# Kernel optimization log

Hardware: AMD Instinct MI355X
Metric: run time of the kernel (lower is better)

Reference implementation:

```python
import jax, jax.numpy as jnp
import numpy as np
import math

T, B, C, F, H, LF, GF = 1024, 8, 512, 64, 8, 64, 64


def setup_inputs() -> dict:
    key = jax.random.key(0)
    ks = jax.random.split(key, 24)
    s = 0.02  # weight init scale for stability through the recurrence
    rn = lambda k, shp, sc=1.0: jax.random.normal(k, shp, jnp.float32) * sc
    inp = {
        "x": rn(ks[0], (B, T, C)),
        "ln_g": jnp.ones((C,), jnp.float32),
        "ln_b": jnp.zeros((C,), jnp.float32),
        "tl_initial": rn(ks[1], (C,)),
        "tl_premix": jax.random.uniform(ks[2], (C,), jnp.float32),
        "tl_w1": rn(ks[3], (C, LF), s), "tl_b1": jnp.zeros((LF,), jnp.float32),
        "tl_w2": rn(ks[4], (LF, C), s), "tl_b2": jnp.zeros((C,), jnp.float32),
        "bias": jnp.zeros((C,), jnp.float32),
        "gating_res": jax.random.uniform(ks[5], (C,), jnp.float32),
        "g_w1": rn(ks[6], (C, GF), s), "g_b1": jnp.zeros((GF,), jnp.float32),
        "g_w2": rn(ks[7], (GF, C), s), "g_b2": jnp.zeros((C,), jnp.float32),
        "dn_initial": rn(ks[8], (H, F, F)),
        "A_w": rn(ks[9], (H, C, F), s), "A_b": rn(ks[10], (H, F), s),
        "B_w": jnp.zeros((H, C, F), jnp.float32), "B_b": rn(ks[11], (H, F), s),
        "C_w": rn(ks[12], (H, C, F), s), "C_b": rn(ks[13], (H, F), s),
        "D_w": rn(ks[14], (H, C, F), s), "D_b": rn(ks[15], (H, F), s),
        "I_w": rn(ks[16], (H, C, F), s), "I_b": rn(ks[17], (H, F), s),
        "S_w": rn(ks[18], (H, C, F), s), "S_b": rn(ks[19], (H, F), s),
        "O_w": rn(ks[20], (H, F, C), s),
    }
    return inp


def _deltanet_head(y, init_state, Aw, Ab, Bw, Bb, Cw, Cb, Dw, Db, Iw, Ib, Sw, Sb, Ow):
    # y: [T, B, C]; init_state: [F, F]
    f = init_state.shape[-1]
    sf = math.sqrt(f)  # awk_safe
    a = y @ Aw + Ab   # [T,B,F]
    b = y @ Bw + Bb
    c = y @ Cw + Cb
    d = y @ Dw + Db
    i = y @ Iw + Ib
    sel = y @ Sw + Sb
    st0 = jnp.broadcast_to(init_state, (y.shape[1], f, f)).astype(y.dtype)

    def step(st, ins):
        sel_t, a_t, b_t, c_t, d_t, i_t = ins  # each [B,F]
        st = (st * jax.nn.sigmoid(i_t)[:, None, :]
              + jnp.einsum('bij,bj->bi', st, a_t)[:, :, None] * b_t[:, None, :] / sf
              + c_t[:, :, None] * d_t[:, None, :])
        out = jnp.einsum('bf,bfg->bg', sel_t, st)
        return st, out

    st, o = jax.lax.scan(step, st0, (sel, a, b, c, d, i))
    return o @ Ow, st  # [T,B,C]


def reference(x, ln_g, ln_b, tl_initial, tl_premix, tl_w1, tl_b1, tl_w2, tl_b2,
              bias, gating_res, g_w1, g_b1, g_w2, g_b2, dn_initial,
              A_w, A_b, B_w, B_b, C_w, C_b, D_w, D_b, I_w, I_b, S_w, S_b, O_w):
    xt = jnp.swapaxes(x, 0, -2)  # [T, B, C] (time_dim=-2)
    res = xt
    # LayerNorm (eps=1e-5)
    mu = jnp.mean(xt, -1, keepdims=True)
    var = jnp.mean((xt - mu) ** 2, -1, keepdims=True)
    h = (xt - mu) / jnp.sqrt(var + 1e-5) * ln_g + ln_b
    # TokenLerp (state=None -> xf[0]=initial)
    xf = jnp.concatenate([jnp.broadcast_to(tl_initial, (1,) + h.shape[1:]).astype(h.dtype), h[:-1]], axis=0)
    pm = h + (xf - h) * tl_premix
    decide = jax.nn.sigmoid(jax.nn.gelu(pm @ tl_w1 + tl_b1, approximate=False) @ tl_w2 + tl_b2)
    h = h + (xf - h) * decide
    # y starts from bias; heads are chained sequentially (y feeds next head)
    y = jnp.broadcast_to(bias, h.shape).astype(h.dtype)
    for k in range(dn_initial.shape[0]):
        y, _ = _deltanet_head(y, dn_initial[k], A_w[k], A_b[k], B_w[k], B_b[k],
                              C_w[k], C_b[k], D_w[k], D_b[k], I_w[k], I_b[k],
                              S_w[k], S_b[k], O_w[k])
    gate = jax.nn.sigmoid(jax.nn.gelu((y + h * gating_res) @ g_w1 + g_b1, approximate=False) @ g_w2 + g_b2)
    # use_residual=True path: returns res + y (no transpose back, matching source)
    return res + y * gate
```

## Files before the change

### kernel.cpp

```cpp
#include <hip/hip_runtime.h>
#include <hip/hip_bf16.h>

#define T_DIM 1024
#define B_DIM 8
#define C_DIM 512
#define F_DIM 64
#define H_DIM 8
#define CHUNK 32
#define NCHUNK 32

__device__ __forceinline__ float sigmoidf_(float v) { return 1.0f / (1.0f + __expf(-v)); }
__device__ __forceinline__ float geluf_(float v) { return 0.5f * v * (1.0f + erff(v * 0.70710678118654752f)); }
__device__ __forceinline__ float rl_(float v, int l) {
  return __uint_as_float(__builtin_amdgcn_readlane(__float_as_uint(v), l));
}

struct GemmArgs {
  const float* A; const float* W; const float* bias; float* out;
  int M, K, N;
  const float* x; const float* mu; const float* rstd;
  const float* ln_g; const float* ln_b; const float* tl_initial; const float* premix;
  const float* yv; const float* gres;
  float* h2;
  const float* Wg[6]; const float* bg[6];
};

struct AFetch {
  float4 v0, v1, v2, v3, v4;
  float s0, s1, s2, s3;
};

template<int MODE_A>
__device__ __forceinline__ AFetch a_fetch(const GemmArgs& g, int r, int c) {
  AFetch f; f.s0 = f.s1 = f.s2 = f.s3 = 0.f;
  if (MODE_A == 0) {
    f.v0 = *(const float4*)&g.A[r * g.K + c];
  } else if (MODE_A == 1) {
    const int b = r & 7, t = r >> 3;
    f.v0 = *(const float4*)&g.x[(b * T_DIM + t) * C_DIM + c];
    f.s0 = g.mu[r]; f.s1 = g.rstd[r];
    if (t > 0) {
      f.v1 = *(const float4*)&g.x[(b * T_DIM + t - 1) * C_DIM + c];
      f.s2 = g.mu[r - 8]; f.s3 = g.rstd[r - 8];
    } else {
      f.v1 = *(const float4*)&g.tl_initial[c];
    }
    f.v2 = *(const float4*)&g.ln_g[c];
    f.v3 = *(const float4*)&g.ln_b[c];
    f.v4 = *(const float4*)&g.premix[c];
  } else {
    f.v0 = *(const float4*)&g.yv[(r >> 3) * C_DIM + c];
    f.v1 = *(const float4*)&g.h2[r * C_DIM + c];
    f.v2 = *(const float4*)&g.gres[c];
  }
  return f;
}

template<int MODE_A>
__device__ __forceinline__ float4 a_combine(const AFetch& f, int r) {
  if (MODE_A == 0) return f.v0;
  float4 o;
  float* op = (float*)&o;
  const float* xa = (const float*)&f.v0;
  const float* xb = (const float*)&f.v1;
  const float* lg = (const float*)&f.v2;
  const float* lb = (const float*)&f.v3;
  const float* pm = (const float*)&f.v4;
  if (MODE_A == 1) {
    const int t = r >> 3;
    #pragma unroll
    for (int q = 0; q < 4; ++q) {
      float h  = (xa[q] - f.s0) * f.s1 * lg[q] + lb[q];
      float xf = (t == 0) ? xb[q] : (xb[q] - f.s2) * f.s3 * lg[q] + lb[q];
      op[q] = h + (xf - h) * pm[q];
    }
    return o;
  }
  #pragma unroll
  for (int q = 0; q < 4; ++q)
    op[q] = xa[q] + xb[q] * lg[q];
  return o;
}

template<int MODE_B>
__device__ __forceinline__ float4 w_fetch(const GemmArgs& g, int kk, int n0, int tc) {
  if (MODE_B == 1)
    return *(const float4*)&g.Wg[blockIdx.y][kk * 64 + (tc << 2)];
  return *(const float4*)&g.W[kk * g.N + n0 + (tc << 2)];
}

template<int MODE_A, int MODE_B, int EPI>
__global__ __launch_bounds__(256) void gemm_kernel(GemmArgs g) {
  __shared__ float AsT[16][68];
  __shared__ float Bs[16][64];
  const int m0 = blockIdx.x * 64, n0 = blockIdx.y * 64;
  const int tid = threadIdx.x;
  const int tr = tid >> 4, tc = tid & 15;
  const int ai = tid >> 2, aj = (tid & 3) << 2;
  const float scg = (MODE_B == 1 && blockIdx.y == 1) ? 0.125f : 1.0f;
  float acc[4][4] = {};
  AFetch fa = a_fetch<MODE_A>(g, m0 + ai, aj);
  float4 wv = w_fetch<MODE_B>(g, tr, n0, tc);
  for (int k0 = 0; k0 < g.K; k0 += 16) {
    if (k0) __syncthreads();
    const float4 av = a_combine<MODE_A>(fa, m0 + ai);
    AsT[aj + 0][ai] = av.x;
    AsT[aj + 1][ai] = av.y;
    AsT[aj + 2][ai] = av.z;
    AsT[aj + 3][ai] = av.w;
    *(float4*)&Bs[tr][tc << 2] =
        make_float4(wv.x * scg, wv.y * scg, wv.z * scg, wv.w * scg);
    if (k0 + 16 < g.K) {
      fa = a_fetch<MODE_A>(g, m0 + ai, k0 + 16 + aj);
      wv = w_fetch<MODE_B>(g, k0 + 16 + tr, n0, tc);
    }
    __syncthreads();
    #pragma unroll
    for (int kk = 0; kk < 16; ++kk) {
      const float4 a4 = *(const float4*)&AsT[kk][tr << 2];
      const float4 b4 = *(const float4*)&Bs[kk][tc << 2];
      const float avr[4] = {a4.x, a4.y, a4.z, a4.w};
      const float bvr[4] = {b4.x, b4.y, b4.z, b4.w};
      #pragma unroll
      for (int r_ = 0; r_ < 4; ++r_)
        #pragma unroll
        for (int c_ = 0; c_ < 4; ++c_)
          acc[r_][c_] = fmaf(avr[r_], bvr[c_], acc[r_][c_]);
    }
  }
  #pragma unroll
  for (int r_ = 0; r_ < 4; ++r_) {
    const int rr = m0 + (tr << 2) + r_;
    #pragma unroll
    for (int c_ = 0; c_ < 4; ++c_) {
      const int lc = (tc << 2) + c_;
      const int cc = n0 + lc;
      float v = acc[r_][c_];
      if (MODE_B == 1) v += g.bg[blockIdx.y][lc] * scg;
      else if (g.bias) v += g.bias[cc];
      if (EPI == 0) {
        g.out[rr * g.N + cc] = v;
      } else if (EPI == 1) {
        g.out[rr * g.N + cc] = geluf_(v);
      } else if (EPI == 2) {
        float d = sigmoidf_(v);
        const int b = rr & 7, t = rr >> 3;
        float xv = g.x[(b * T_DIM + t) * C_DIM + cc];
        float h = (xv - g.mu[rr]) * g.rstd[rr] * g.ln_g[cc] + g.ln_b[cc];
        float xf;
        if (t == 0) xf = g.tl_initial[cc];
        else {
          float xp = g.x[(b * T_DIM + t - 1) * C_DIM + cc];
          xf = (xp - g.mu[rr - 8]) * g.rstd[rr - 8] * g.ln_g[cc] + g.ln_b[cc];
        }
        g.h2[rr * C_DIM + cc] = h + (xf - h) * d;
      } else {
        float gate = sigmoidf_(v);
        const int b = rr & 7, t = rr >> 3;
        float res = g.x[(b * T_DIM + t) * C_DIM + cc];
        g.out[rr * C_DIM + cc] = res + g.yv[t * C_DIM + cc] * gate;
      }
    }
  }
}

__global__ __launch_bounds__(256) void ln_stats_kernel(const float* __restrict__ x,
                                                       float* __restrict__ mu,
                                                       float* __restrict__ rstd) {
  const int row = blockIdx.x * 4 + (threadIdx.x >> 6);
  const int lane = threadIdx.x & 63;
  const int b = row & 7, t = row >> 3;
  const float* xr = x + (b * T_DIM + t) * C_DIM;
  float4 v0 = *(const float4*)&xr[lane * 8];
  float4 v1 = *(const float4*)&xr[lane * 8 + 4];
  float s  = v0.x + v0.y + v0.z + v0.w + v1.x + v1.y + v1.z + v1.w;
  float s2 = v0.x*v0.x + v0.y*v0.y + v0.z*v0.z + v0.w*v0.w
           + v1.x*v1.x + v1.y*v1.y + v1.z*v1.z + v1.w*v1.w;
  #pragma unroll
  for (int m = 1; m < 64; m <<= 1) { s += __shfl_xor(s, m); s2 += __shfl_xor(s2, m); }
  if (lane == 0) {
    float mean = s * (1.0f / 512.0f);
    float var = s2 * (1.0f / 512.0f) - mean * mean;
    mu[row] = mean;
    rstd[row] = rsqrtf(var + 1e-5f);
  }
}

__global__ __launch_bounds__(256) void yinit_kernel(const float* __restrict__ bias,
                                                    float* __restrict__ y) {
  int i = blockIdx.x * blockDim.x + threadIdx.x;
  y[i] = bias[i & (C_DIM - 1)];
}


__global__ __launch_bounds__(256) void scan_phaseA(const float* __restrict__ PRJ,
                                                   float* __restrict__ chPT,
                                                   float* __restrict__ chS) {
  const int j = blockIdx.x;
  const int tid = threadIdx.x;
  const int ri = tid >> 4, ci = tid & 15;
  float Pm[4][4], Sm[4][4];
  #pragma unroll
  for (int r = 0; r < 4; ++r)
    #pragma unroll
    for (int c = 0; c < 4; ++c) {
      Pm[r][c] = (ri * 4 + r == ci * 4 + c) ? 1.0f : 0.0f;
      Sm[r][c] = 0.0f;
    }
  const float* base = PRJ + j * CHUNK * 384;
  float4 pa = *(const float4*)&base[      ci * 4];
  float4 pb = *(const float4*)&base[ 64 + ci * 4];
  float4 pc = *(const float4*)&base[128 + ri * 4];
  float4 pd = *(const float4*)&base[192 + ci * 4];
  float4 pi = *(const float4*)&base[256 + ci * 4];
  for (int s = 0; s < CHUNK; ++s) {
    float4 na = pa, nb = pb, nc2 = pc, nd = pd, ni = pi;
    if (s + 1 < CHUNK) {
      const float* b2 = base + (s + 1) * 384;
      na  = *(const float4*)&b2[      ci * 4];
      nb  = *(const float4*)&b2[ 64 + ci * 4];
      nc2 = *(const float4*)&b2[128 + ri * 4];
      nd  = *(const float4*)&b2[192 + ci * 4];
      ni  = *(const float4*)&b2[256 + ci * 4];
    }
    const float sg[4] = {sigmoidf_(pi.x), sigmoidf_(pi.y), sigmoidf_(pi.z), sigmoidf_(pi.w)};
    const float aa[4] = {pa.x, pa.y, pa.z, pa.w};
    const float bb[4] = {pb.x, pb.y, pb.z, pb.w};
    const float cv[4] = {pc.x, pc.y, pc.z, pc.w};
    const float dd[4] = {pd.x, pd.y, pd.z, pd.w};
    float rp[4], rs[4];
    #pragma unroll
    for (int r = 0; r < 4; ++r) {
      rp[r] = Pm[r][0]*aa[0] + Pm[r][1]*aa[1] + Pm[r][2]*aa[2] + Pm[r][3]*aa[3];
      rs[r] = Sm[r][0]*aa[0] + Sm[r][1]*aa[1] + Sm[r][2]*aa[2] + Sm[r][3]*aa[3];
    }
    #pragma unroll
    for (int m = 1; m <= 8; m <<= 1) {
      #pragma unroll
      for (int r = 0; r < 4; ++r) {
        rp[r] += __shfl_xor(rp[r], m);
        rs[r] += __shfl_xor(rs[r], m);
      }
    }
    #pragma unroll
    for (int r = 0; r < 4; ++r)
      #pragma unroll
      for (int c = 0; c < 4; ++c) {
        Pm[r][c] = Pm[r][c] * sg[c] + rp[r] * bb[c];
        Sm[r][c] = Sm[r][c] * sg[c] + rs[r] * bb[c] + cv[r] * dd[c];
      }
    pa = na; pb = nb; pc = nc2; pd = nd; pi = ni;
  }
  float* cpT = chPT + j * 4096;
  float* cs  = chS + j * 4096;
  #pragma unroll
  for (int c = 0; c < 4; ++c)
    *(float4*)&cpT[(ci*4+c)*64 + ri*4] =
        make_float4(Pm[0][c], Pm[1][c], Pm[2][c], Pm[3][c]);
  #pragma unroll
  for (int r = 0; r < 4; ++r)
    *(float4*)&cs[(ri*4+r)*64 + ci*4] = make_float4(Sm[r][0], Sm[r][1], Sm[r][2], Sm[r][3]);
}

__device__ __forceinline__ float cstep(const float4 (&P)[16], float sv, float rv) {
  float p0 = 0.f, p1 = 0.f, p2 = 0.f, p3 = 0.f;
  #pragma unroll
  for (int q = 0; q < 16; ++q) {
    p0 = fmaf(rl_(rv, q * 4 + 0), P[q].x, p0);
    p1 = fmaf(rl_(rv, q * 4 + 1), P[q].y, p1);
    p2 = fmaf(rl_(rv, q * 4 + 2), P[q].z, p2);
    p3 = fmaf(rl_(rv, q * 4 + 3), P[q].w, p3);
  }
  return sv + ((p0 + p1) + (p2 + p3));
}

__global__ __launch_bounds__(64) void scan_combine(const float* __restrict__ st0,
                                                   const float* __restrict__ chPT,
                                                   const float* __restrict__ chS,
                                                   float* __restrict__ bnd) {
  const int lane = threadIdx.x;
  const int r = blockIdx.x;
  float rv = st0[r * 64 + lane];
  const float* basePT = chPT + lane * 64;
  const float* baseS  = chS + r * 64 + lane;
  float* bndRL = bnd + r * 64 + lane;
  for (int j = 0; j < NCHUNK; ++j) {
    float4 P[16];
    const float* pp = basePT + j * 4096;
    #pragma unroll
    for (int q = 0; q < 16; ++q) P[q] = *(const float4*)&pp[q * 4];
    const float sv = baseS[j * 4096];
    bndRL[j * 4096] = rv;
    rv = cstep(P, sv, rv);
  }
}

__global__ __launch_bounds__(256) void scan_phaseC(const float* __restrict__ PRJ,
                                                   const float* __restrict__ bnd,
                                                   const float* __restrict__ Ow,
                                                   float* __restrict__ y) {
  __shared__ float olds[CHUNK][4][64];
  __shared__ float osT[64][CHUNK + 1];
  const int j = blockIdx.x;
  const int tid = threadIdx.x;
  const int ri = tid >> 4, ci = tid & 15, w = tid >> 6;
  float st[4][4];
  #pragma unroll
  for (int r = 0; r < 4; ++r) {
    const float4 v = *(const float4*)&bnd[j*4096 + (ri*4+r)*64 + ci*4];
    st[r][0] = v.x; st[r][1] = v.y; st[r][2] = v.z; st[r][3] = v.w;
  }
  const float* base = PRJ + j * CHUNK * 384;
  float4 pa = *(const float4*)&base[      ci * 4];
  float4 pb = *(const float4*)&base[ 64 + ci * 4];
  float4 pc = *(const float4*)&base[128 + ri * 4];
  float4 pd = *(const float4*)&base[192 + ci * 4];
  float4 pi = *(const float4*)&base[256 + ci * 4];
  float4 ps = *(const float4*)&base[320 + ri * 4];
  for (int s = 0; s < CHUNK; ++s) {
    float4 na = pa, nb = pb, nc2 = pc, nd = pd, ni = pi, ns = ps;
    if (s + 1 < CHUNK) {
      const float* b2 = base + (s + 1) * 384;
      na  = *(const float4*)&b2[      ci * 4];
      nb  = *(const float4*)&b2[ 64 + ci * 4];
      nc2 = *(const float4*)&b2[128 + ri * 4];
      nd  = *(const float4*)&b2[192 + ci * 4];
      ni  = *(const float4*)&b2[256 + ci * 4];
      ns  = *(const float4*)&b2[320 + ri * 4];
    }
    const float sg[4] = {sigmoidf_(pi.x), sigmoidf_(pi.y), sigmoidf_(pi.z), sigmoidf_(pi.w)};
    const float aa[4] = {pa.x, pa.y, pa.z, pa.w};
    const float bb[4] = {pb.x, pb.y, pb.z, pb.w};
    const float cv[4] = {pc.x, pc.y, pc.z, pc.w};
    const float dd[4] = {pd.x, pd.y, pd.z, pd.w};
    const float ss[4] = {ps.x, ps.y, ps.z, ps.w};
    float rd[4];
    #pragma unroll
    for (int r = 0; r < 4; ++r)
      rd[r] = st[r][0]*aa[0] + st[r][1]*aa[1] + st[r][2]*aa[2] + st[r][3]*aa[3];
    #pragma unroll
    for (int m = 1; m <= 8; m <<= 1) {
      #pragma unroll
      for (int r = 0; r < 4; ++r) rd[r] += __shfl_xor(rd[r], m);
    }
    float po[4] = {0.f, 0.f, 0.f, 0.f};
    #pragma unroll
    for (int r = 0; r < 4; ++r)
      #pragma unroll
      for (int c = 0; c < 4; ++c) {
        const float nv = st[r][c] * sg[c] + rd[r] * bb[c] + cv[r] * dd[c];
        st[r][c] = nv;
        po[c] = fmaf(ss[r], nv, po[c]);
      }
    #pragma unroll
    for (int c = 0; c < 4; ++c) {
      po[c] += __shfl_xor(po[c], 16);
      po[c] += __shfl_xor(po[c], 32);
    }
    if ((tid & 48) == 0)
      *(float4*)&olds[s][w][ci * 4] = make_float4(po[0], po[1], po[2], po[3]);
    pa = na; pb = nb; pc = nc2; pd = nd; pi = ni; ps = ns;
  }
  __syncthreads();
  #pragma unroll
  for (int e = 0; e < 8; ++e) {
    const int id = tid + 256 * e;
    const int f = id & 63, t = id >> 6;
    osT[f][t] = olds[t][0][f] + olds[t][1][f] + olds[t][2][f] + olds[t][3][f];
  }
  __syncthreads();
  const int c0 = tid << 1;
  float2 acc[CHUNK];
  #pragma unroll
  for (int t = 0; t < CHUNK; ++t) acc[t] = make_float2(0.f, 0.f);
  #pragma unroll 1
  for (int fo = 0; fo < 8; ++fo) {
    float2 ow[8];
    #pragma unroll
    for (int q = 0; q < 8; ++q)
      ow[q] = *(const float2*)&Ow[(fo * 8 + q) * C_DIM + c0];
    #pragma unroll
    for (int q = 0; q < 8; ++q) {
      const int f = fo * 8 + q;
      #pragma unroll
      for (int t8 = 0; t8 < 8; ++t8) {
        const float4 ov = *(const float4*)&osT[f][t8 * 4];
        acc[t8*4+0].x = fmaf(ov.x, ow[q].x, acc[t8*4+0].x);
        acc[t8*4+0].y = fmaf(ov.x, ow[q].y, acc[t8*4+0].y);
        acc[t8*4+1].x = fmaf(ov.y, ow[q].x, acc[t8*4+1].x);
        acc[t8*4+1].y = fmaf(ov.y, ow[q].y, acc[t8*4+1].y);
        acc[t8*4+2].x = fmaf(ov.z, ow[q].x, acc[t8*4+2].x);
        acc[t8*4+2].y = fmaf(ov.z, ow[q].y, acc[t8*4+2].y);
        acc[t8*4+3].x = fmaf(ov.w, ow[q].x, acc[t8*4+3].x);
        acc[t8*4+3].y = fmaf(ov.w, ow[q].y, acc[t8*4+3].y);
      }
    }
  }
  #pragma unroll
  for (int t = 0; t < CHUNK; ++t)
    *(float2*)&y[(j * CHUNK + t) * C_DIM + c0] = acc[t];
}

extern "C" void kernel_launch(void* const* d_in, const int* in_sizes, int n_in,
                              void* d_out, int out_size, void* d_ws, size_t ws_size,
                              hipStream_t stream) {
  const float* x       = (const float*)d_in[0];
  const float* ln_g    = (const float*)d_in[1];
  const float* ln_b    = (const float*)d_in[2];
  const float* tl_init = (const float*)d_in[3];
  const float* premix  = (const float*)d_in[4];
  const float* tl_w1   = (const float*)d_in[5];
  const float* tl_b1   = (const float*)d_in[6];
  const float* tl_w2   = (const float*)d_in[7];
  const float* tl_b2   = (const float*)d_in[8];
  const float* bias    = (const float*)d_in[9];
  const float* gres    = (const float*)d_in[10];
  const float* g_w1    = (const float*)d_in[11];
  const float* g_b1    = (const float*)d_in[12];
  const float* g_w2    = (const float*)d_in[13];
  const float* g_b2    = (const float*)d_in[14];
  const float* dn_init = (const float*)d_in[15];
  const float* A_w     = (const float*)d_in[16];
  const float* A_b     = (const float*)d_in[17];
  const float* B_w     = (const float*)d_in[18];
  const float* B_b     = (const float*)d_in[19];
  const float* C_w     = (const float*)d_in[20];
  const float* C_b     = (const float*)d_in[21];
  const float* D_w     = (const float*)d_in[22];
  const float* D_b     = (const float*)d_in[23];
  const float* I_w     = (const float*)d_in[24];
  const float* I_b     = (const float*)d_in[25];
  const float* S_w     = (const float*)d_in[26];
  const float* S_b     = (const float*)d_in[27];
  const float* O_w     = (const float*)d_in[28];

  float* ws      = (float*)d_ws;
  float* mu      = ws;
  float* rstd    = mu + 8192;
  float* hidden1 = rstd + 8192;
  float* y       = hidden1 + 524288;
  float* PRJ     = y + 524288;
  float* chPT    = PRJ + 393216;
  float* chS     = chPT + 131072;
  float* bnd     = chS + 131072;
  float* h2      = (float*)d_out;

  ln_stats_kernel<<<2048, 256, 0, stream>>>(x, mu, rstd);
  yinit_kernel<<<2048, 256, 0, stream>>>(bias, y);

  GemmArgs ga = {};
  ga.x = x; ga.mu = mu; ga.rstd = rstd; ga.ln_g = ln_g; ga.ln_b = ln_b;
  ga.tl_initial = tl_init; ga.premix = premix; ga.gres = gres; ga.h2 = h2;

  {
    GemmArgs g = ga; g.W = tl_w1; g.bias = tl_b1; g.out = hidden1;
    g.M = 8192; g.K = 512; g.N = 64;
    gemm_kernel<1, 0, 1><<<dim3(128, 1), 256, 0, stream>>>(g);
  }
  {
    GemmArgs g = ga; g.A = hidden1; g.W = tl_w2; g.bias = tl_b2;
    g.M = 8192; g.K = 64; g.N = 512;
    gemm_kernel<0, 0, 2><<<dim3(128, 8), 256, 0, stream>>>(g);
  }

  for (int k = 0; k < H_DIM; ++k) {
    {
      GemmArgs g = ga; g.A = y; g.out = PRJ; g.M = 1024; g.K = 512; g.N = 384;
      const int woff = k * C_DIM * F_DIM, boff = k * F_DIM;
      g.Wg[0] = A_w + woff; g.Wg[1] = B_w + woff; g.Wg[2] = C_w + woff;
      g.Wg[3] = D_w + woff; g.Wg[4] = I_w + woff; g.Wg[5] = S_w + woff;
      g.bg[0] = A_b + boff; g.bg[1] = B_b + boff; g.bg[2] = C_b + boff;
      g.bg[3] = D_b + boff; g.bg[4] = I_b + boff; g.bg[5] = S_b + boff;
      gemm_kernel<0, 1, 0><<<dim3(16, 6), 256, 0, stream>>>(g);
    }
    scan_phaseA<<<NCHUNK, 256, 0, stream>>>(PRJ, chPT, chS);
    scan_combine<<<64, 64, 0, stream>>>(dn_init + k * 4096, chPT, chS, bnd);
    scan_phaseC<<<NCHUNK, 256, 0, stream>>>(PRJ, bnd, O_w + k * F_DIM * C_DIM, y);
  }

  {
    GemmArgs g = ga; g.yv = y; g.W = g_w1; g.bias = g_b1; g.out = hidden1;
    g.M = 8192; g.K = 512; g.N = 64;
    gemm_kernel<2, 0, 1><<<dim3(128, 1), 256, 0, stream>>>(g);
  }
  {
    GemmArgs g = ga; g.yv = y; g.A = hidden1; g.W = g_w2; g.bias = g_b2;
    g.out = (float*)d_out; g.M = 8192; g.K = 64; g.N = 512;
    gemm_kernel<0, 0, 3><<<dim3(128, 8), 256, 0, stream>>>(g);
  }
}
```

Before: 968.0 us.

## Fuse MLP GEMM pairs, fuse head projection into scan phase A, merge y init

The two-layer MLPs (token-lerp decide and output gate) now run as one kernel per MLP. The 64-wide hidden activation stays in shared memory and each block loops over all 512 output columns, which removes the hidden1 round trip and a launch. Each head's projection GEMM is folded into scan_phaseA, so every chunk block computes its own 32x384 projections into LDS before scanning. The y bias initialization is merged into ln_stats. The cost is that projection now runs on only 32 blocks instead of 96, and the second MLP GEMM runs on 128 blocks instead of 1024, which lowers parallelism.

```diff
diff --git a/kernel.cpp b/kernel.cpp
--- a/kernel.cpp
+++ b/kernel.cpp
@@ -16,13 +16,12 @@
 }
 
 struct GemmArgs {
-  const float* A; const float* W; const float* bias; float* out;
-  int M, K, N;
+  const float* W; const float* bias; const float* W2; const float* bias2;
+  float* out;
   const float* x; const float* mu; const float* rstd;
   const float* ln_g; const float* ln_b; const float* tl_initial; const float* premix;
   const float* yv; const float* gres;
   float* h2;
-  const float* Wg[6]; const float* bg[6];
 };
 
 struct AFetch {
@@ -33,9 +32,7 @@
 template<int MODE_A>
 __device__ __forceinline__ AFetch a_fetch(const GemmArgs& g, int r, int c) {
   AFetch f; f.s0 = f.s1 = f.s2 = f.s3 = 0.f;
-  if (MODE_A == 0) {
-    f.v0 = *(const float4*)&g.A[r * g.K + c];
-  } else if (MODE_A == 1) {
+  if (MODE_A == 1) {
     const int b = r & 7, t = r >> 3;
     f.v0 = *(const float4*)&g.x[(b * T_DIM + t) * C_DIM + c];
     f.s0 = g.mu[r]; f.s1 = g.rstd[r];
@@ -58,7 +55,6 @@
 
 template<int MODE_A>
 __device__ __forceinline__ float4 a_combine(const AFetch& f, int r) {
-  if (MODE_A == 0) return f.v0;
   float4 o;
   float* op = (float*)&o;
   const float* xa = (const float*)&f.v0;
@@ -82,43 +78,61 @@
   return o;
 }
 
-template<int MODE_B>
-__device__ __forceinline__ float4 w_fetch(const GemmArgs& g, int kk, int n0, int tc) {
-  if (MODE_B == 1)
-    return *(const float4*)&g.Wg[blockIdx.y][kk * 64 + (tc << 2)];
-  return *(const float4*)&g.W[kk * g.N + n0 + (tc << 2)];
-}
-
-template<int MODE_A, int MODE_B, int EPI>
-__global__ __launch_bounds__(256) void gemm_kernel(GemmArgs g) {
+template<int MODE_A, int EPI>
+__global__ __launch_bounds__(256) void mlp_fused_kernel(GemmArgs g) {
   __shared__ float AsT[16][68];
   __shared__ float Bs[16][64];
-  const int m0 = blockIdx.x * 64, n0 = blockIdx.y * 64;
+  __shared__ float hT[64][68];
+  const int m0 = blockIdx.x * 64;
   const int tid = threadIdx.x;
   const int tr = tid >> 4, tc = tid & 15;
   const int ai = tid >> 2, aj = (tid & 3) << 2;
-  const float scg = (MODE_B == 1 && blockIdx.y == 1) ? 0.125f : 1.0f;
-  float acc[4][4] = {};
-  AFetch fa = a_fetch<MODE_A>(g, m0 + ai, aj);
-  float4 wv = w_fetch<MODE_B>(g, tr, n0, tc);
-  for (int k0 = 0; k0 < g.K; k0 += 16) {
-    if (k0) __syncthreads();
-    const float4 av = a_combine<MODE_A>(fa, m0 + ai);
-    AsT[aj + 0][ai] = av.x;
-    AsT[aj + 1][ai] = av.y;
-    AsT[aj + 2][ai] = av.z;
-    AsT[aj + 3][ai] = av.w;
-    *(float4*)&Bs[tr][tc << 2] =
-        make_float4(wv.x * scg, wv.y * scg, wv.z * scg, wv.w * scg);
-    if (k0 + 16 < g.K) {
-      fa = a_fetch<MODE_A>(g, m0 + ai, k0 + 16 + aj);
-      wv = w_fetch<MODE_B>(g, k0 + 16 + tr, n0, tc);
+  {
+    float acc[4][4] = {};
+    AFetch fa = a_fetch<MODE_A>(g, m0 + ai, aj);
+    float4 wv = *(const float4*)&g.W[tr * 64 + (tc << 2)];
+    for (int k0 = 0; k0 < 512; k0 += 16) {
+      if (k0) __syncthreads();
+      const float4 av = a_combine<MODE_A>(fa, m0 + ai);
+      AsT[aj + 0][ai] = av.x;
+      AsT[aj + 1][ai] = av.y;
+      AsT[aj + 2][ai] = av.z;
+      AsT[aj + 3][ai] = av.w;
+      *(float4*)&Bs[tr][tc << 2] = wv;
+      if (k0 + 16 < 512) {
+        fa = a_fetch<MODE_A>(g, m0 + ai, k0 + 16 + aj);
+        wv = *(const float4*)&g.W[(k0 + 16 + tr) * 64 + (tc << 2)];
+      }
+      __syncthreads();
+      #pragma unroll
+      for (int kk = 0; kk < 16; ++kk) {
+        const float4 a4 = *(const float4*)&AsT[kk][tr << 2];
+        const float4 b4 = *(const float4*)&Bs[kk][tc << 2];
+        const float avr[4] = {a4.x, a4.y, a4.z, a4.w};
+        const float bvr[4] = {b4.x, b4.y, b4.z, b4.w};
+        #pragma unroll
+        for (int r_ = 0; r_ < 4; ++r_)
+          #pragma unroll
+          for (int c_ = 0; c_ < 4; ++c_)
+            acc[r_][c_] = fmaf(avr[r_], bvr[c_], acc[r_][c_]);
+      }
     }
     __syncthreads();
     #pragma unroll
-    for (int kk = 0; kk < 16; ++kk) {
-      const float4 a4 = *(const float4*)&AsT[kk][tr << 2];
-      const float4 b4 = *(const float4*)&Bs[kk][tc << 2];
+    for (int r_ = 0; r_ < 4; ++r_)
+      #pragma unroll
+      for (int c_ = 0; c_ < 4; ++c_) {
+        const int cc = (tc << 2) + c_;
+        hT[cc][(tr << 2) + r_] = geluf_(acc[r_][c_] + g.bias[cc]);
+      }
+  }
+  __syncthreads();
+  for (int n0 = 0; n0 < 512; n0 += 64) {
+    float acc[4][4] = {};
+    #pragma unroll 4
+    for (int kk = 0; kk < 64; ++kk) {
+      const float4 a4 = *(const float4*)&hT[kk][tr << 2];
+      const float4 b4 = *(const float4*)&g.W2[kk * 512 + n0 + (tc << 2)];
       const float avr[4] = {a4.x, a4.y, a4.z, a4.w};
       const float bvr[4] = {b4.x, b4.y, b4.z, b4.w};
       #pragma unroll
@@ -127,38 +141,31 @@
         for (int c_ = 0; c_ < 4; ++c_)
           acc[r_][c_] = fmaf(avr[r_], bvr[c_], acc[r_][c_]);
     }
-  }
-  #pragma unroll
-  for (int r_ = 0; r_ < 4; ++r_) {
-    const int rr = m0 + (tr << 2) + r_;
-    #pragma unroll
-    for (int c_ = 0; c_ < 4; ++c_) {
-      const int lc = (tc << 2) + c_;
-      const int cc = n0 + lc;
-      float v = acc[r_][c_];
-      if (MODE_B == 1) v += g.bg[blockIdx.y][lc] * scg;
-      else if (g.bias) v += g.bias[cc];
-      if (EPI == 0) {
-        g.out[rr * g.N + cc] = v;
-      } else if (EPI == 1) {
-        g.out[rr * g.N + cc] = geluf_(v);
-      } else if (EPI == 2) {
-        float d = sigmoidf_(v);
-        const int b = rr & 7, t = rr >> 3;
-        float xv = g.x[(b * T_DIM + t) * C_DIM + cc];
-        float h = (xv - g.mu[rr]) * g.rstd[rr] * g.ln_g[cc] + g.ln_b[cc];
-        float xf;
-        if (t == 0) xf = g.tl_initial[cc];
-        else {
-          float xp = g.x[(b * T_DIM + t - 1) * C_DIM + cc];
-          xf = (xp - g.mu[rr - 8]) * g.rstd[rr - 8] * g.ln_g[cc] + g.ln_b[cc];
+    #pragma unroll
+    for (int r_ = 0; r_ < 4; ++r_) {
+      const int rr = m0 + (tr << 2) + r_;
+      #pragma unroll
+      for (int c_ = 0; c_ < 4; ++c_) {
+        const int cc = n0 + (tc << 2) + c_;
+        float v = acc[r_][c_] + g.bias2[cc];
+        if (EPI == 2) {
+          float d = sigmoidf_(v);
+          const int b = rr & 7, t = rr >> 3;
+          float xv = g.x[(b * T_DIM + t) * C_DIM + cc];
+          float h = (xv - g.mu[rr]) * g.rstd[rr] * g.ln_g[cc] + g.ln_b[cc];
+          float xf;
+          if (t == 0) xf = g.tl_initial[cc];
+          else {
+            float xp = g.x[(b * T_DIM + t - 1) * C_DIM + cc];
+            xf = (xp - g.mu[rr - 8]) * g.rstd[rr - 8] * g.ln_g[cc] + g.ln_b[cc];
+          }
+          g.h2[rr * C_DIM + cc] = h + (xf - h) * d;
+        } else {
+          float gate = sigmoidf_(v);
+          const int b = rr & 7, t = rr >> 3;
+          float res = g.x[(b * T_DIM + t) * C_DIM + cc];
+          g.out[rr * C_DIM + cc] = res + g.yv[t * C_DIM + cc] * gate;
         }
-        g.h2[rr * C_DIM + cc] = h + (xf - h) * d;
-      } else {
-        float gate = sigmoidf_(v);
-        const int b = rr & 7, t = rr >> 3;
-        float res = g.x[(b * T_DIM + t) * C_DIM + cc];
-        g.out[rr * C_DIM + cc] = res + g.yv[t * C_DIM + cc] * gate;
       }
     }
   }
@@ -166,7 +173,11 @@
 
 __global__ __launch_bounds__(256) void ln_stats_kernel(const float* __restrict__ x,
                                                        float* __restrict__ mu,
-                                                       float* __restrict__ rstd) {
+                                                       float* __restrict__ rstd,
+                                                       const float* __restrict__ bias,
+                                                       float* __restrict__ y) {
+  const int gid = blockIdx.x * 256 + threadIdx.x;
+  y[gid] = bias[gid & (C_DIM - 1)];
   const int row = blockIdx.x * 4 + (threadIdx.x >> 6);
   const int lane = threadIdx.x & 63;
   const int b = row & 7, t = row >> 3;
@@ -186,18 +197,62 @@
   }
 }
 
-__global__ __launch_bounds__(256) void yinit_kernel(const float* __restrict__ bias,
-                                                    float* __restrict__ y) {
-  int i = blockIdx.x * blockDim.x + threadIdx.x;
-  y[i] = bias[i & (C_DIM - 1)];
-}
-
-
-__global__ __launch_bounds__(256) void scan_phaseA(const float* __restrict__ PRJ,
-                                                   float* __restrict__ chPT,
-                                                   float* __restrict__ chS) {
+
+struct ProjAArgs {
+  const float* y; float* PRJ; float* chPT; float* chS;
+  const float* Wg[6]; const float* bg[6];
+};
+
+__global__ __launch_bounds__(256) void projA_kernel(ProjAArgs a) {
+  __shared__ float prjS[32][388];
+  __shared__ float ys[16][36];
+  __shared__ float Bs2[16][64];
   const int j = blockIdx.x;
+  const int R0 = j * CHUNK;
   const int tid = threadIdx.x;
+  {
+    const int rq = tid >> 5, ct = tid & 31;
+    const int srow = tid >> 3, sfq = tid & 7;
+    const int wkk = tid >> 4, wc4 = (tid & 15) << 2;
+    for (int grp = 0; grp < 6; ++grp) {
+      const float* W = a.Wg[grp];
+      const float scg = (grp == 1) ? 0.125f : 1.0f;
+      float acc[4][2] = {};
+      for (int k0 = 0; k0 < 512; k0 += 16) {
+        if (sfq < 4) {
+          const float4 v = *(const float4*)&a.y[(R0 + srow) * C_DIM + k0 + sfq * 4];
+          ys[sfq * 4 + 0][srow] = v.x; ys[sfq * 4 + 1][srow] = v.y;
+          ys[sfq * 4 + 2][srow] = v.z; ys[sfq * 4 + 3][srow] = v.w;
+        }
+        const float4 wv = *(const float4*)&W[(k0 + wkk) * 64 + wc4];
+        *(float4*)&Bs2[wkk][wc4] =
+            make_float4(wv.x * scg, wv.y * scg, wv.z * scg, wv.w * scg);
+        __syncthreads();
+        #pragma unroll
+        for (int kk = 0; kk < 16; ++kk) {
+          const float4 a4 = *(const float4*)&ys[kk][rq << 2];
+          const float2 b2 = *(const float2*)&Bs2[kk][ct << 1];
+          const float avr[4] = {a4.x, a4.y, a4.z, a4.w};
+          #pragma unroll
+          for (int r_ = 0; r_ < 4; ++r_) {
+            acc[r_][0] = fmaf(avr[r_], b2.x, acc[r_][0]);
+            acc[r_][1] = fmaf(avr[r_], b2.y, acc[r_][1]);
+          }
+        }
+        __syncthreads();
+      }
+      const float* bb = a.bg[grp];
+      const float b0 = bb[ct * 2] * scg, b1 = bb[ct * 2 + 1] * scg;
+      #pragma unroll
+      for (int r_ = 0; r_ < 4; ++r_) {
+        const int row = rq * 4 + r_;
+        const float2 o = make_float2(acc[r_][0] + b0, acc[r_][1] + b1);
+        *(float2*)&prjS[row][grp * 64 + ct * 2] = o;
+        *(float2*)&a.PRJ[(R0 + row) * 384 + grp * 64 + ct * 2] = o;
+      }
+      __syncthreads();
+    }
+  }
   const int ri = tid >> 4, ci = tid & 15;
   float Pm[4][4], Sm[4][4];
   #pragma unroll
@@ -207,25 +262,15 @@
       Pm[r][c] = (ri * 4 + r == ci * 4 + c) ? 1.0f : 0.0f;
       Sm[r][c] = 0.0f;
     }
-  const float* base = PRJ + j * CHUNK * 384;
-  float4 pa = *(const float4*)&base[      ci * 4];
-  float4 pb = *(const float4*)&base[ 64 + ci * 4];
-  float4 pc = *(const float4*)&base[128 + ri * 4];
-  float4 pd = *(const float4*)&base[192 + ci * 4];
-  float4 pi = *(const float4*)&base[256 + ci * 4];
   for (int s = 0; s < CHUNK; ++s) {
-    float4 na = pa, nb = pb, nc2 = pc, nd = pd, ni = pi;
-    if (s + 1 < CHUNK) {
-      const float* b2 = base + (s + 1) * 384;
-      na  = *(const float4*)&b2[      ci * 4];
-      nb  = *(const float4*)&b2[ 64 + ci * 4];
-      nc2 = *(const float4*)&b2[128 + ri * 4];
-      nd  = *(const float4*)&b2[192 + ci * 4];
-      ni  = *(const float4*)&b2[256 + ci * 4];
-    }
+    const float4 pa = *(const float4*)&prjS[s][      ci * 4];
+    const float4 pb = *(const float4*)&prjS[s][ 64 + ci * 4];
+    const float4 pc = *(const float4*)&prjS[s][128 + ri * 4];
+    const float4 pd = *(const float4*)&prjS[s][192 + ci * 4];
+    const float4 pi = *(const float4*)&prjS[s][256 + ci * 4];
     const float sg[4] = {sigmoidf_(pi.x), sigmoidf_(pi.y), sigmoidf_(pi.z), sigmoidf_(pi.w)};
     const float aa[4] = {pa.x, pa.y, pa.z, pa.w};
-    const float bb[4] = {pb.x, pb.y, pb.z, pb.w};
+    const float bb2[4] = {pb.x, pb.y, pb.z, pb.w};
     const float cv[4] = {pc.x, pc.y, pc.z, pc.w};
     const float dd[4] = {pd.x, pd.y, pd.z, pd.w};
     float rp[4], rs[4];
@@ -246,13 +291,12 @@
     for (int r = 0; r < 4; ++r)
       #pragma unroll
       for (int c = 0; c < 4; ++c) {
-        Pm[r][c] = Pm[r][c] * sg[c] + rp[r] * bb[c];
-        Sm[r][c] = Sm[r][c] * sg[c] + rs[r] * bb[c] + cv[r] * dd[c];
-      }
-    pa = na; pb = nb; pc = nc2; pd = nd; pi = ni;
-  }
-  float* cpT = chPT + j * 4096;
-  float* cs  = chS + j * 4096;
+        Pm[r][c] = Pm[r][c] * sg[c] + rp[r] * bb2[c];
+        Sm[r][c] = Sm[r][c] * sg[c] + rs[r] * bb2[c] + cv[r] * dd[c];
+      }
+  }
+  float* cpT = a.chPT + j * 4096;
+  float* cs  = a.chS + j * 4096;
   #pragma unroll
   for (int c = 0; c < 4; ++c)
     *(float4*)&cpT[(ci*4+c)*64 + ri*4] =
@@ -330,7 +374,7 @@
     }
     const float sg[4] = {sigmoidf_(pi.x), sigmoidf_(pi.y), sigmoidf_(pi.z), sigmoidf_(pi.w)};
     const float aa[4] = {pa.x, pa.y, pa.z, pa.w};
-    const float bb[4] = {pb.x, pb.y, pb.z, pb.w};
+    const float bb2[4] = {pb.x, pb.y, pb.z, pb.w};
     const float cv[4] = {pc.x, pc.y, pc.z, pc.w};
     const float dd[4] = {pd.x, pd.y, pd.z, pd.w};
     const float ss[4] = {ps.x, ps.y, ps.z, ps.w};
@@ -348,7 +392,7 @@
     for (int r = 0; r < 4; ++r)
       #pragma unroll
       for (int c = 0; c < 4; ++c) {
-        const float nv = st[r][c] * sg[c] + rd[r] * bb[c] + cv[r] * dd[c];
+        const float nv = st[r][c] * sg[c] + rd[r] * bb2[c] + cv[r] * dd[c];
         st[r][c] = nv;
         po[c] = fmaf(ss[r], nv, po[c]);
       }
@@ -437,55 +481,42 @@
   float* ws      = (float*)d_ws;
   float* mu      = ws;
   float* rstd    = mu + 8192;
-  float* hidden1 = rstd + 8192;
-  float* y       = hidden1 + 524288;
+  float* y       = rstd + 8192;
   float* PRJ     = y + 524288;
   float* chPT    = PRJ + 393216;
   float* chS     = chPT + 131072;
   float* bnd     = chS + 131072;
   float* h2      = (float*)d_out;
 
-  ln_stats_kernel<<<2048, 256, 0, stream>>>(x, mu, rstd);
-  yinit_kernel<<<2048, 256, 0, stream>>>(bias, y);
+  ln_stats_kernel<<<2048, 256, 0, stream>>>(x, mu, rstd, bias, y);
 
   GemmArgs ga = {};
   ga.x = x; ga.mu = mu; ga.rstd = rstd; ga.ln_g = ln_g; ga.ln_b = ln_b;
   ga.tl_initial = tl_init; ga.premix = premix; ga.gres = gres; ga.h2 = h2;
 
   {
-    GemmArgs g = ga; g.W = tl_w1; g.bias = tl_b1; g.out = hidden1;
-    g.M = 8192; g.K = 512; g.N = 64;
-    gemm_kernel<1, 0, 1><<<dim3(128, 1), 256, 0, stream>>>(g);
-  }
-  {
-    GemmArgs g = ga; g.A = hidden1; g.W = tl_w2; g.bias = tl_b2;
-    g.M = 8192; g.K = 64; g.N = 512;
-    gemm_kernel<0, 0, 2><<<dim3(128, 8), 256, 0, stream>>>(g);
+    GemmArgs g = ga; g.W = tl_w1; g.bias = tl_b1; g.W2 = tl_w2; g.bias2 = tl_b2;
+    mlp_fused_kernel<1, 2><<<128, 256, 0, stream>>>(g);
   }
 
   for (int k = 0; k < H_DIM; ++k) {
     {
-      GemmArgs g = ga; g.A = y; g.out = PRJ; g.M = 1024; g.K = 512; g.N = 384;
+      ProjAArgs pa;
+      pa.y = y; pa.PRJ = PRJ; pa.chPT = chPT; pa.chS = chS;
       const int woff = k * C_DIM * F_DIM, boff = k * F_DIM;
-      g.Wg[0] = A_w + woff; g.Wg[1] = B_w + woff; g.Wg[2] = C_w + woff;
-      g.Wg[3] = D_w + woff; g.Wg[4] = I_w + woff; g.Wg[5] = S_w + woff;
-      g.bg[0] = A_b + boff; g.bg[1] = B_b + boff; g.bg[2] = C_b + boff;
-      g.bg[3] = D_b + boff; g.bg[4] = I_b + boff; g.bg[5] = S_b + boff;
-      gemm_kernel<0, 1, 0><<<dim3(16, 6), 256, 0, stream>>>(g);
-    }
-    scan_phaseA<<<NCHUNK, 256, 0, stream>>>(PRJ, chPT, chS);
+      pa.Wg[0] = A_w + woff; pa.Wg[1] = B_w + woff; pa.Wg[2] = C_w + woff;
+      pa.Wg[3] = D_w + woff; pa.Wg[4] = I_w + woff; pa.Wg[5] = S_w + woff;
+      pa.bg[0] = A_b + boff; pa.bg[1] = B_b + boff; pa.bg[2] = C_b + boff;
+      pa.bg[3] = D_b + boff; pa.bg[4] = I_b + boff; pa.bg[5] = S_b + boff;
+      projA_kernel<<<NCHUNK, 256, 0, stream>>>(pa);
+    }
     scan_combine<<<64, 64, 0, stream>>>(dn_init + k * 4096, chPT, chS, bnd);
     scan_phaseC<<<NCHUNK, 256, 0, stream>>>(PRJ, bnd, O_w + k * F_DIM * C_DIM, y);
   }
 
   {
-    GemmArgs g = ga; g.yv = y; g.W = g_w1; g.bias = g_b1; g.out = hidden1;
-    g.M = 8192; g.K = 512; g.N = 64;
-    gemm_kernel<2, 0, 1><<<dim3(128, 1), 256, 0, stream>>>(g);
-  }
-  {
-    GemmArgs g = ga; g.yv = y; g.A = hidden1; g.W = g_w2; g.bias = g_b2;
-    g.out = (float*)d_out; g.M = 8192; g.K = 64; g.N = 512;
-    gemm_kernel<0, 0, 3><<<dim3(128, 8), 256, 0, stream>>>(g);
-  }
-}
+    GemmArgs g = ga; g.yv = y; g.W = g_w1; g.bias = g_b1; g.W2 = g_w2; g.bias2 = g_b2;
+    g.out = (float*)d_out;
+    mlp_fused_kernel<2, 3><<<128, 256, 0, stream>>>(g);
+  }
+}
```

After: 2.072 ms. +114.0%, slower.
